# Kernel optimization log

Measured on AMD Instinct MI355X. Metric: run time of the kernel, lower is better.

The kernel has to match this reference:

```python
import jax, jax.numpy as jnp
import numpy as np
import math

SLEEP_DIM = 1024
BRAIN_DIM = 512
N_HEADS = 8
D_K = SLEEP_DIM // N_HEADS
N_S = 2048
N_C = 4096
LN_EPS = 1e-5


def setup_inputs() -> dict:
    key = jax.random.key(0)
    ks = jax.random.split(key, 9)
    s = 0.02  # weight init scale
    return {
        "H_S": jax.random.normal(ks[0], (N_S, SLEEP_DIM), dtype=jnp.float32),
        "H_C": jax.random.normal(ks[1], (N_C, BRAIN_DIM), dtype=jnp.float32),
        "G_glyph": jax.random.uniform(ks[2], (N_S, N_C), dtype=jnp.float32),
        "W_Q": jax.random.normal(ks[3], (SLEEP_DIM, SLEEP_DIM), dtype=jnp.float32) * s,
        "W_K": jax.random.normal(ks[4], (SLEEP_DIM, BRAIN_DIM), dtype=jnp.float32) * s,
        "W_V": jax.random.normal(ks[5], (SLEEP_DIM, BRAIN_DIM), dtype=jnp.float32) * s,
        "W_O": jax.random.normal(ks[6], (SLEEP_DIM, SLEEP_DIM), dtype=jnp.float32) * s,
        "b_O": jnp.zeros((SLEEP_DIM,), dtype=jnp.float32),
        "ln_gamma": jnp.ones((SLEEP_DIM,), dtype=jnp.float32),
        "ln_beta": jnp.zeros((SLEEP_DIM,), dtype=jnp.float32),
    }


def reference(H_S, H_C, G_glyph, W_Q, W_K, W_V, W_O, b_O, ln_gamma, ln_beta):
    # projections (torch Linear: x @ W.T)
    Q = (H_S @ W_Q.T).reshape(N_S, N_HEADS, D_K)   # (N_S, H, d_k)
    K = (H_C @ W_K.T).reshape(N_C, N_HEADS, D_K)   # (N_C, H, d_k)
    V = (H_C @ W_V.T).reshape(N_C, N_HEADS, D_K)   # (N_C, H, d_k)

    # scores: (N_S, N_C, H), scaled then multiplicatively gated per (s, c) pair
    scores = jnp.einsum("shd,chd->sch", Q, K) / math.sqrt(D_K)
    scores = scores * G_glyph[:, :, None]

    # softmax over keys (dim=1 of (N_S, N_C, H)); dropout is identity at eval
    attn = jax.nn.softmax(scores, axis=1)

    # weighted value sum, merge heads
    H_new = jnp.einsum("sch,chd->shd", attn, V).reshape(N_S, SLEEP_DIM)
    H_new = H_new @ W_O.T + b_O

    # residual + LayerNorm
    x = H_new + H_S
    mu = jnp.mean(x, axis=-1, keepdims=True)
    var = jnp.var(x, axis=-1, keepdims=True)
    out = (x - mu) / jnp.sqrt(var + LN_EPS) * ln_gamma + ln_beta
    return out, attn.mean(-1)
```

## Files before the change

### kernel.cpp

```cpp
#include <hip/hip_runtime.h>
#include <hip/hip_bf16.h>

#define NS 2048
#define NC 4096
#define SD 1024
#define BD 512
#define NH 8
#define DK 128

typedef __bf16 bf16;
typedef __bf16 bf16x8 __attribute__((ext_vector_type(8)));
typedef __bf16 bf16x4 __attribute__((ext_vector_type(4)));
typedef float f32x4 __attribute__((ext_vector_type(4)));

__device__ __forceinline__ bf16 f2bf(float f) { return (bf16)f; }
__device__ __forceinline__ bf16x8 ld8(const bf16* p) { return *(const bf16x8*)p; }
__device__ __forceinline__ f32x4 mfma16(bf16x8 a, bf16x8 b, f32x4 c) {
  return __builtin_amdgcn_mfma_f32_16x16x32_bf16(a, b, c, 0, 0, 0);
}

__global__ void k_cast(const float* __restrict__ in, bf16* __restrict__ out, int n4) {
  int i = blockIdx.x * blockDim.x + threadIdx.x;
  int stride = gridDim.x * blockDim.x;
  for (; i < n4; i += stride) {
    float4 v = ((const float4*)in)[i];
    bf16x4 o;
    o[0] = f2bf(v.x); o[1] = f2bf(v.y); o[2] = f2bf(v.z); o[3] = f2bf(v.w);
    ((bf16x4*)out)[i] = o;
  }
}

template <typename CT>
__global__ __launch_bounds__(256) void k_gemm_bt(const bf16* __restrict__ A,
                                                 const bf16* __restrict__ B,
                                                 CT* __restrict__ C,
                                                 int M, int N, int K) {
  __shared__ bf16 As[128 * 64];
  __shared__ bf16 Bs[64 * 64];
  const int tid = threadIdx.x;
  const int l = tid & 63, w = tid >> 6;
  const int g = l >> 4, r15 = l & 15;
  const int m0 = blockIdx.y * 128, n0 = blockIdx.x * 64;
  const int wm = (w >> 1) * 64, wn = (w & 1) * 32;
  f32x4 acc[4][2] = {};
  for (int k0 = 0; k0 < K; k0 += 64) {
    __syncthreads();
#pragma unroll
    for (int i = 0; i < 4; i++) {
      int slot = tid + i * 256;
      int row = slot >> 3, cp = slot & 7;
      int gc = cp ^ (row & 7);
      *(uint4*)(As + slot * 8) = *(const uint4*)(A + (size_t)(m0 + row) * K + k0 + gc * 8);
    }
#pragma unroll
    for (int i = 0; i < 2; i++) {
      int slot = tid + i * 256;
      int row = slot >> 3, cp = slot & 7;
      int gc = cp ^ (row & 7);
      *(uint4*)(Bs + slot * 8) = *(const uint4*)(B + (size_t)(n0 + row) * K + k0 + gc * 8);
    }
    __syncthreads();
#pragma unroll
    for (int kk = 0; kk < 2; kk++) {
      bf16x8 af[4], bfr[2];
#pragma unroll
      for (int mi = 0; mi < 4; mi++) {
        int row = wm + mi * 16 + r15;
        int cidx = (kk * 4 + g) ^ (row & 7);
        af[mi] = *(const bf16x8*)(As + row * 64 + cidx * 8);
      }
#pragma unroll
      for (int ni = 0; ni < 2; ni++) {
        int row = wn + ni * 16 + r15;
        int cidx = (kk * 4 + g) ^ (row & 7);
        bfr[ni] = *(const bf16x8*)(Bs + row * 64 + cidx * 8);
      }
#pragma unroll
      for (int mi = 0; mi < 4; mi++)
#pragma unroll
        for (int ni = 0; ni < 2; ni++)
          acc[mi][ni] = mfma16(af[mi], bfr[ni], acc[mi][ni]);
    }
  }
#pragma unroll
  for (int mi = 0; mi < 4; mi++)
#pragma unroll
    for (int ni = 0; ni < 2; ni++)
#pragma unroll
      for (int rr = 0; rr < 4; rr++) {
        int mrow = m0 + wm + mi * 16 + g * 4 + rr;
        int ncol = n0 + wn + ni * 16 + r15;
        float v = acc[mi][ni][rr];
        if constexpr (sizeof(CT) == 4) C[(size_t)mrow * N + ncol] = v;
        else                           C[(size_t)mrow * N + ncol] = f2bf(v);
      }
}

__global__ __launch_bounds__(256) void k_transpose(const bf16* __restrict__ V, bf16* __restrict__ Vt) {
  __shared__ bf16 tile[32][33];
  const int t = threadIdx.x;
  const int col = t & 31, r0 = t >> 5;
  const int cbase = blockIdx.y * 32;
  const int dbase = blockIdx.x * 32;
#pragma unroll
  for (int i = 0; i < 4; i++) {
    int r = r0 + i * 8;
    tile[r][col] = V[(size_t)(cbase + r) * SD + dbase + col];
  }
  __syncthreads();
#pragma unroll
  for (int i = 0; i < 4; i++) {
    int r = r0 + i * 8;
    Vt[(size_t)(dbase + r) * NC + cbase + col] = tile[col][r];
  }
}

__global__ __launch_bounds__(256) void k_attn2(const bf16* __restrict__ Q, const bf16* __restrict__ Km,
                                               const bf16* __restrict__ Vt, const float* __restrict__ Gf,
                                               float* __restrict__ psum_part, bf16* __restrict__ Opart) {
  __shared__ bf16 Kl[64 * 128];
  __shared__ bf16 Vl[128 * 64];
  __shared__ bf16 Pl[4][32 * 64];
  const int tid = threadIdx.x;
  const int l = tid & 63, w = tid >> 6;
  const int g = l >> 4, r15 = l & 15;
  const int s0 = blockIdx.x * 128;
  const int h = blockIdx.y, hoff = h * DK;
  const int ch = blockIdx.z;
  const int cbase = ch * (NC / 4);
  const float scale = 0.08838834764831845f;
  char* KlB = (char*)Kl;
  char* VlB = (char*)Vl;
  char* PlB = (char*)Pl[w];
  const int swz = r15 & 7;

  bf16x8 qf[2][4];
#pragma unroll
  for (int smi = 0; smi < 2; smi++)
#pragma unroll
    for (int kk = 0; kk < 4; kk++)
      qf[smi][kk] = ld8(Q + (size_t)(s0 + w * 32 + smi * 16 + r15) * SD + hoff + kk * 32 + g * 8);

  f32x4 oacc[8][2] = {};
  float psum[2] = {0.f, 0.f};

  const int krow0 = tid >> 4, ksl = tid & 15;
  const int vrow0 = tid >> 3, vsl = tid & 7;

  uint4 kreg[4], vreg[4];
  auto loadstep = [&](int cb) {
#pragma unroll
    for (int i = 0; i < 4; i++)
      kreg[i] = *(const uint4*)(Km + (size_t)(cb + krow0 + i * 16) * SD + hoff + ksl * 8);
#pragma unroll
    for (int i = 0; i < 4; i++)
      vreg[i] = *(const uint4*)(Vt + (size_t)(hoff + vrow0 + i * 32) * NC + cb + vsl * 8);
  };
  loadstep(cbase);

  for (int t = 0; t < 16; ++t) {
    const int cb = cbase + t * 64;
    __syncthreads();
#pragma unroll
    for (int i = 0; i < 4; i++) {
      int row = krow0 + i * 16;
      *(uint4*)(KlB + row * 256 + ((ksl ^ (row & 7)) << 4)) = kreg[i];
    }
#pragma unroll
    for (int i = 0; i < 4; i++) {
      int row = vrow0 + i * 32;
      *(uint4*)(VlB + row * 128 + ((vsl ^ (row & 7)) << 4)) = vreg[i];
    }
    __syncthreads();
    if (t < 15) loadstep(cb + 64);
#pragma unroll
    for (int csub = 0; csub < 4; ++csub) {
      bf16x8 kf[4];
#pragma unroll
      for (int kk = 0; kk < 4; kk++)
        kf[kk] = *(const bf16x8*)(KlB + (csub * 16 + r15) * 256 + (((kk * 4 + g) ^ swz) << 4));
#pragma unroll
      for (int smi = 0; smi < 2; smi++) {
        f32x4 a = {0.f, 0.f, 0.f, 0.f};
#pragma unroll
        for (int kk = 0; kk < 4; kk++) a = mfma16(kf[kk], qf[smi][kk], a);
        const int srow = s0 + w * 32 + smi * 16 + r15;
        float4 gv = *(const float4*)(Gf + (size_t)srow * NC + cb + csub * 16 + g * 4);
        float p0 = __expf(a[0] * scale * gv.x);
        float p1 = __expf(a[1] * scale * gv.y);
        float p2 = __expf(a[2] * scale * gv.z);
        float p3 = __expf(a[3] * scale * gv.w);
        psum[smi] += (p0 + p1) + (p2 + p3);
        bf16 pk[4] __attribute__((aligned(8)));
        pk[0] = f2bf(p0); pk[1] = f2bf(p1); pk[2] = f2bf(p2); pk[3] = f2bf(p3);
        *(uint2*)(PlB + (smi * 16 + r15) * 128 + ((csub * 32 + g * 8) ^ (swz << 4))) = *(const uint2*)pk;
      }
    }
#pragma unroll
    for (int kc = 0; kc < 2; ++kc) {
      bf16x8 pf[2];
#pragma unroll
      for (int smi = 0; smi < 2; smi++)
        pf[smi] = *(const bf16x8*)(PlB + (smi * 16 + r15) * 128 + ((kc * 64 + g * 16) ^ (swz << 4)));
#pragma unroll
      for (int nf = 0; nf < 8; ++nf) {
        bf16x8 vf = *(const bf16x8*)(VlB + (nf * 16 + r15) * 128 + (((kc * 4 + g) ^ swz) << 4));
#pragma unroll
        for (int smi = 0; smi < 2; smi++)
          oacc[nf][smi] = mfma16(vf, pf[smi], oacc[nf][smi]);
      }
    }
  }
#pragma unroll
  for (int smi = 0; smi < 2; smi++) {
    float ps = psum[smi];
    ps += __shfl_xor(ps, 16);
    ps += __shfl_xor(ps, 32);
    if (g == 0) {
      int srow = s0 + w * 32 + smi * 16 + r15;
      psum_part[((size_t)ch * NS + srow) * NH + h] = ps;
    }
  }
#pragma unroll
  for (int nf = 0; nf < 8; nf++)
#pragma unroll
    for (int smi = 0; smi < 2; smi++) {
      int srow = s0 + w * 32 + smi * 16 + r15;
      bf16 ob[4] __attribute__((aligned(8)));
#pragma unroll
      for (int rr = 0; rr < 4; rr++) ob[rr] = f2bf(oacc[nf][smi][rr]);
      *(uint2*)(Opart + ((size_t)ch * NS + srow) * SD + hoff + nf * 16 + g * 4) = *(const uint2*)ob;
    }
}

__global__ __launch_bounds__(256) void k_combine(const float* __restrict__ psum_part,
                                                 const bf16* __restrict__ Opart,
                                                 bf16* __restrict__ Hat, float* __restrict__ inv_l) {
  __shared__ float il_s[NH];
  const int row = blockIdx.x, t = threadIdx.x;
  if (t < NH) {
    float s = 0.f;
#pragma unroll
    for (int ch = 0; ch < 4; ch++) s += psum_part[((size_t)ch * NS + row) * NH + t];
    float iv = 1.0f / s;
    il_s[t] = iv;
    inv_l[(size_t)row * NH + t] = iv;
  }
  __syncthreads();
  const int d0 = t * 4;
  float acc[4] = {0.f, 0.f, 0.f, 0.f};
#pragma unroll
  for (int ch = 0; ch < 4; ch++) {
    bf16x4 v = *(const bf16x4*)(Opart + ((size_t)ch * NS + row) * SD + d0);
#pragma unroll
    for (int j = 0; j < 4; j++) acc[j] += (float)v[j];
  }
  float iv = il_s[d0 >> 7];
  bf16 ob[4] __attribute__((aligned(8)));
#pragma unroll
  for (int j = 0; j < 4; j++) ob[j] = f2bf(acc[j] * iv);
  *(uint2*)(Hat + (size_t)row * SD + d0) = *(const uint2*)ob;
}

__global__ __launch_bounds__(256) void k_mean2(const bf16* __restrict__ Q, const bf16* __restrict__ Km,
                                               const float* __restrict__ Gf, const float* __restrict__ inv_l,
                                               float* __restrict__ out_mean) {
  __shared__ bf16 Klm[64 * 128];
  __shared__ bf16 Qlm[64 * 128];
  const int tid = threadIdx.x;
  const int l = tid & 63, w = tid >> 6;
  const int g = l >> 4, r15 = l & 15;
  const int ws = w >> 1, wc = w & 1;
  const int c0 = blockIdx.x * 64, s0 = blockIdx.y * 64;
  const float scale = 0.08838834764831845f;
  const int swz = r15 & 7;
  char* KB = (char*)Klm;
  char* QB = (char*)Qlm;
  const int row0 = tid >> 4, sl = tid & 15;

  float4 gv[2][2];
#pragma unroll
  for (int smi = 0; smi < 2; smi++)
#pragma unroll
    for (int csub = 0; csub < 2; csub++)
      gv[smi][csub] = *(const float4*)(Gf + (size_t)(s0 + ws * 32 + smi * 16 + r15) * NC +
                                       c0 + wc * 32 + csub * 16 + g * 4);

  f32x4 macc[2][2] = {};
  uint4 kreg[4], qreg[4];
  auto loadh = [&](int h) {
#pragma unroll
    for (int i = 0; i < 4; i++)
      kreg[i] = *(const uint4*)(Km + (size_t)(c0 + row0 + i * 16) * SD + h * DK + sl * 8);
#pragma unroll
    for (int i = 0; i < 4; i++)
      qreg[i] = *(const uint4*)(Q + (size_t)(s0 + row0 + i * 16) * SD + h * DK + sl * 8);
  };
  loadh(0);
  for (int h = 0; h < NH; ++h) {
    __syncthreads();
#pragma unroll
    for (int i = 0; i < 4; i++) {
      int row = row0 + i * 16;
      *(uint4*)(KB + row * 256 + ((sl ^ (row & 7)) << 4)) = kreg[i];
    }
#pragma unroll
    for (int i = 0; i < 4; i++) {
      int row = row0 + i * 16;
      *(uint4*)(QB + row * 256 + ((sl ^ (row & 7)) << 4)) = qreg[i];
    }
    __syncthreads();
    if (h < NH - 1) loadh(h + 1);
    bf16x8 kf[2][4], qfr[2][4];
#pragma unroll
    for (int csub = 0; csub < 2; csub++)
#pragma unroll
      for (int kk = 0; kk < 4; kk++)
        kf[csub][kk] = *(const bf16x8*)(KB + (wc * 32 + csub * 16 + r15) * 256 + (((kk * 4 + g) ^ swz) << 4));
#pragma unroll
    for (int smi = 0; smi < 2; smi++)
#pragma unroll
      for (int kk = 0; kk < 4; kk++)
        qfr[smi][kk] = *(const bf16x8*)(QB + (ws * 32 + smi * 16 + r15) * 256 + (((kk * 4 + g) ^ swz) << 4));
    float ilv[2];
#pragma unroll
    for (int smi = 0; smi < 2; smi++)
      ilv[smi] = inv_l[(size_t)(s0 + ws * 32 + smi * 16 + r15) * NH + h];
#pragma unroll
    for (int smi = 0; smi < 2; smi++)
#pragma unroll
      for (int csub = 0; csub < 2; csub++) {
        f32x4 a = {0.f, 0.f, 0.f, 0.f};
#pragma unroll
        for (int kk = 0; kk < 4; kk++) a = mfma16(kf[csub][kk], qfr[smi][kk], a);
        float4 gvv = gv[smi][csub];
        macc[smi][csub][0] += __expf(a[0] * scale * gvv.x) * ilv[smi];
        macc[smi][csub][1] += __expf(a[1] * scale * gvv.y) * ilv[smi];
        macc[smi][csub][2] += __expf(a[2] * scale * gvv.z) * ilv[smi];
        macc[smi][csub][3] += __expf(a[3] * scale * gvv.w) * ilv[smi];
      }
  }
#pragma unroll
  for (int smi = 0; smi < 2; smi++)
#pragma unroll
    for (int csub = 0; csub < 2; csub++) {
      int srow = s0 + ws * 32 + smi * 16 + r15;
      float4 o;
      o.x = macc[smi][csub][0] * 0.125f;
      o.y = macc[smi][csub][1] * 0.125f;
      o.z = macc[smi][csub][2] * 0.125f;
      o.w = macc[smi][csub][3] * 0.125f;
      *(float4*)(out_mean + (size_t)srow * NC + c0 + wc * 32 + csub * 16 + g * 4) = o;
    }
}

__global__ __launch_bounds__(256) void k_ln(const float* __restrict__ Op, const float* __restrict__ HS,
                                            const float* __restrict__ bO, const float* __restrict__ gamma,
                                            const float* __restrict__ beta, float* __restrict__ out) {
  __shared__ float rs[4][2];
  const int row = blockIdx.x, t = threadIdx.x;
  const int l = t & 63, w = t >> 6;
  float4 xo = *(const float4*)(Op + (size_t)row * SD + t * 4);
  float4 hs = *(const float4*)(HS + (size_t)row * SD + t * 4);
  float4 bo = *(const float4*)(bO + t * 4);
  float x[4] = {xo.x + hs.x + bo.x, xo.y + hs.y + bo.y,
                xo.z + hs.z + bo.z, xo.w + hs.w + bo.w};
  float s = x[0] + x[1] + x[2] + x[3];
  float q = x[0] * x[0] + x[1] * x[1] + x[2] * x[2] + x[3] * x[3];
#pragma unroll
  for (int m = 1; m < 64; m <<= 1) { s += __shfl_xor(s, m); q += __shfl_xor(q, m); }
  if (l == 0) { rs[w][0] = s; rs[w][1] = q; }
  __syncthreads();
  s = rs[0][0] + rs[1][0] + rs[2][0] + rs[3][0];
  q = rs[0][1] + rs[1][1] + rs[2][1] + rs[3][1];
  float mean = s * (1.0f / SD);
  float var = q * (1.0f / SD) - mean * mean;
  float rstd = rsqrtf(var + 1e-5f);
  float4 gm = *(const float4*)(gamma + t * 4);
  float4 bt = *(const float4*)(beta + t * 4);
  float4 o;
  o.x = (x[0] - mean) * rstd * gm.x + bt.x;
  o.y = (x[1] - mean) * rstd * gm.y + bt.y;
  o.z = (x[2] - mean) * rstd * gm.z + bt.z;
  o.w = (x[3] - mean) * rstd * gm.w + bt.w;
  *(float4*)(out + (size_t)row * SD + t * 4) = o;
}

extern "C" void kernel_launch(void* const* d_in, const int* in_sizes, int n_in,
                              void* d_out, int out_size, void* d_ws, size_t ws_size,
                              hipStream_t stream) {
  const float* H_S = (const float*)d_in[0];
  const float* H_C = (const float*)d_in[1];
  const float* G   = (const float*)d_in[2];
  const float* W_Q = (const float*)d_in[3];
  const float* W_K = (const float*)d_in[4];
  const float* W_V = (const float*)d_in[5];
  const float* W_O = (const float*)d_in[6];
  const float* b_O = (const float*)d_in[7];
  const float* gam = (const float*)d_in[8];
  const float* bet = (const float*)d_in[9];
  float* out = (float*)d_out;
  float* out_mean = out + (size_t)NS * SD;

  char* p = (char*)d_ws;
  auto alloc = [&](size_t bytes) { char* r = p; p += (bytes + 255) & ~(size_t)255; return r; };
  char* region0 = alloc((size_t)20 << 20);
  bf16* HSb = (bf16*)region0;
  bf16* HCb = (bf16*)(region0 + ((size_t)4 << 20));
  bf16* WQb = (bf16*)(region0 + ((size_t)8 << 20));
  bf16* WKb = (bf16*)(region0 + ((size_t)10 << 20));
  bf16* WVb = (bf16*)(region0 + ((size_t)11 << 20));
  bf16* Vb  = (bf16*)(region0 + ((size_t)12 << 20));
  bf16* Opart = (bf16*)region0;
  bf16* WOb = (bf16*)alloc((size_t)SD * SD * 2);
  bf16* Qb  = (bf16*)alloc((size_t)NS * SD * 2);
  bf16* Kb  = (bf16*)alloc((size_t)NC * SD * 2);
  bf16* Vtb = (bf16*)alloc((size_t)SD * NC * 2);
  bf16* Hat = (bf16*)alloc((size_t)NS * SD * 2);
  float* Opj = (float*)alloc((size_t)NS * SD * 4);
  float* invl = (float*)alloc((size_t)NS * NH * 4);
  float* psum_part = (float*)alloc((size_t)4 * NS * NH * 4);

  k_cast<<<1024, 256, 0, stream>>>(H_S, HSb, NS * SD / 4);
  k_cast<<<1024, 256, 0, stream>>>(H_C, HCb, NC * BD / 4);
  k_cast<<<1024, 256, 0, stream>>>(W_Q, WQb, SD * SD / 4);
  k_cast<<<1024, 256, 0, stream>>>(W_K, WKb, SD * BD / 4);
  k_cast<<<1024, 256, 0, stream>>>(W_V, WVb, SD * BD / 4);
  k_cast<<<1024, 256, 0, stream>>>(W_O, WOb, SD * SD / 4);

  k_gemm_bt<bf16><<<dim3(SD / 64, NS / 128), 256, 0, stream>>>(HSb, WQb, Qb, NS, SD, SD);
  k_gemm_bt<bf16><<<dim3(SD / 64, NC / 128), 256, 0, stream>>>(HCb, WKb, Kb, NC, SD, BD);
  k_gemm_bt<bf16><<<dim3(SD / 64, NC / 128), 256, 0, stream>>>(HCb, WVb, Vb, NC, SD, BD);
  k_transpose<<<dim3(SD / 32, NC / 32), 256, 0, stream>>>(Vb, Vtb);

  k_attn2<<<dim3(NS / 128, NH, 4), 256, 0, stream>>>(Qb, Kb, Vtb, G, psum_part, Opart);
  k_combine<<<NS, 256, 0, stream>>>(psum_part, Opart, Hat, invl);
  k_mean2<<<dim3(NC / 64, NS / 64), 256, 0, stream>>>(Qb, Kb, G, invl, out_mean);

  k_gemm_bt<float><<<dim3(SD / 64, NS / 128), 256, 0, stream>>>(Hat, WOb, Opj, NS, SD, SD);
  k_ln<<<NS, 256, 0, stream>>>(Opj, H_S, b_O, gam, bet, out);
}
```

Baseline: 516.0 us.

## Fuse casts, cast G to bf16, shrink GEMM tiles, register-shuffle P in attention

Merges all input casts into one kernel and also casts the gating matrix G to bf16, so the attention and mean kernels read half the bytes for G. GEMM tiles shrink from 128x64 to 64x64 to give the grid more blocks. The attention kernel now has each wave handle 16 query rows, and it rearranges P into MFMA operand layout with cross-lane shuffles instead of an LDS round trip. Its output is staged through LDS so global stores are coalesced, and the mean kernel caches inv_l in shared memory. Rounding G to bf16 adds error to the gated scores, and the extra cast pass over G costs a full read of it plus a write of the bf16 copy.

Result: no change. 516.0 us (+0.0%).

```diff
diff --git a/kernel.cpp b/kernel.cpp
--- a/kernel.cpp
+++ b/kernel.cpp
@@ -7,46 +7,81 @@
 #define BD 512
 #define NH 8
 #define DK 128
+#define CSPLIT 4
 
 typedef __bf16 bf16;
 typedef __bf16 bf16x8 __attribute__((ext_vector_type(8)));
 typedef __bf16 bf16x4 __attribute__((ext_vector_type(4)));
 typedef float f32x4 __attribute__((ext_vector_type(4)));
+typedef unsigned u32x4 __attribute__((ext_vector_type(4)));
 
 __device__ __forceinline__ bf16 f2bf(float f) { return (bf16)f; }
 __device__ __forceinline__ bf16x8 ld8(const bf16* p) { return *(const bf16x8*)p; }
 __device__ __forceinline__ f32x4 mfma16(bf16x8 a, bf16x8 b, f32x4 c) {
   return __builtin_amdgcn_mfma_f32_16x16x32_bf16(a, b, c, 0, 0, 0);
 }
-
-__global__ void k_cast(const float* __restrict__ in, bf16* __restrict__ out, int n4) {
+__device__ __forceinline__ unsigned pkbf(float lo, float hi) {
+  unsigned short a = __builtin_bit_cast(unsigned short, (bf16)lo);
+  unsigned short b = __builtin_bit_cast(unsigned short, (bf16)hi);
+  return (unsigned)a | ((unsigned)b << 16);
+}
+
+__global__ void k_cast_all(const float* __restrict__ HS, const float* __restrict__ HC,
+                           const float* __restrict__ WQ, const float* __restrict__ WK,
+                           const float* __restrict__ WV, const float* __restrict__ WO,
+                           const float* __restrict__ G,
+                           bf16* __restrict__ HSb, bf16* __restrict__ HCb,
+                           bf16* __restrict__ WQb, bf16* __restrict__ WKb,
+                           bf16* __restrict__ WVb, bf16* __restrict__ WOb,
+                           bf16* __restrict__ Gb) {
+  const int n0 = NS * SD / 4, n1 = NC * BD / 4, n2 = SD * SD / 4, n3 = SD * BD / 4;
+  const int n4 = SD * BD / 4, n5 = SD * SD / 4, n6 = NS * NC / 4;
+  const int total = n0 + n1 + n2 + n3 + n4 + n5 + n6;
   int i = blockIdx.x * blockDim.x + threadIdx.x;
-  int stride = gridDim.x * blockDim.x;
-  for (; i < n4; i += stride) {
-    float4 v = ((const float4*)in)[i];
+  const int stride = gridDim.x * blockDim.x;
+  for (; i < total; i += stride) {
+    const float* s; bf16* d; int off = i;
+    if (off < n0) { s = HS; d = HSb; }
+    else { off -= n0;
+      if (off < n1) { s = HC; d = HCb; }
+      else { off -= n1;
+        if (off < n2) { s = WQ; d = WQb; }
+        else { off -= n2;
+          if (off < n3) { s = WK; d = WKb; }
+          else { off -= n3;
+            if (off < n4) { s = WV; d = WVb; }
+            else { off -= n4;
+              if (off < n5) { s = WO; d = WOb; }
+              else { off -= n5; s = G; d = Gb; }
+            }
+          }
+        }
+      }
+    }
+    float4 v = ((const float4*)s)[off];
     bf16x4 o;
     o[0] = f2bf(v.x); o[1] = f2bf(v.y); o[2] = f2bf(v.z); o[3] = f2bf(v.w);
-    ((bf16x4*)out)[i] = o;
+    ((bf16x4*)d)[off] = o;
   }
 }
 
 template <typename CT>
-__global__ __launch_bounds__(256) void k_gemm_bt(const bf16* __restrict__ A,
-                                                 const bf16* __restrict__ B,
-                                                 CT* __restrict__ C,
-                                                 int M, int N, int K) {
-  __shared__ bf16 As[128 * 64];
+__global__ __launch_bounds__(256) void k_gemm64(const bf16* __restrict__ A,
+                                                const bf16* __restrict__ B,
+                                                CT* __restrict__ C,
+                                                int M, int N, int K) {
+  __shared__ bf16 As[64 * 64];
   __shared__ bf16 Bs[64 * 64];
   const int tid = threadIdx.x;
   const int l = tid & 63, w = tid >> 6;
   const int g = l >> 4, r15 = l & 15;
-  const int m0 = blockIdx.y * 128, n0 = blockIdx.x * 64;
-  const int wm = (w >> 1) * 64, wn = (w & 1) * 32;
-  f32x4 acc[4][2] = {};
+  const int m0 = blockIdx.y * 64, n0 = blockIdx.x * 64;
+  const int wm = (w >> 1) * 32, wn = (w & 1) * 32;
+  f32x4 acc[2][2] = {};
   for (int k0 = 0; k0 < K; k0 += 64) {
     __syncthreads();
 #pragma unroll
-    for (int i = 0; i < 4; i++) {
+    for (int i = 0; i < 2; i++) {
       int slot = tid + i * 256;
       int row = slot >> 3, cp = slot & 7;
       int gc = cp ^ (row & 7);
@@ -62,9 +97,9 @@
     __syncthreads();
 #pragma unroll
     for (int kk = 0; kk < 2; kk++) {
-      bf16x8 af[4], bfr[2];
-#pragma unroll
-      for (int mi = 0; mi < 4; mi++) {
+      bf16x8 af[2], bfr[2];
+#pragma unroll
+      for (int mi = 0; mi < 2; mi++) {
         int row = wm + mi * 16 + r15;
         int cidx = (kk * 4 + g) ^ (row & 7);
         af[mi] = *(const bf16x8*)(As + row * 64 + cidx * 8);
@@ -76,14 +111,14 @@
         bfr[ni] = *(const bf16x8*)(Bs + row * 64 + cidx * 8);
       }
 #pragma unroll
-      for (int mi = 0; mi < 4; mi++)
+      for (int mi = 0; mi < 2; mi++)
 #pragma unroll
         for (int ni = 0; ni < 2; ni++)
           acc[mi][ni] = mfma16(af[mi], bfr[ni], acc[mi][ni]);
     }
   }
 #pragma unroll
-  for (int mi = 0; mi < 4; mi++)
+  for (int mi = 0; mi < 2; mi++)
 #pragma unroll
     for (int ni = 0; ni < 2; ni++)
 #pragma unroll
@@ -115,38 +150,31 @@
   }
 }
 
-__global__ __launch_bounds__(256) void k_attn2(const bf16* __restrict__ Q, const bf16* __restrict__ Km,
-                                               const bf16* __restrict__ Vt, const float* __restrict__ Gf,
-                                               float* __restrict__ psum_part, bf16* __restrict__ Opart) {
+__global__ __launch_bounds__(256, 4) void k_attn3(const bf16* __restrict__ Q, const bf16* __restrict__ Km,
+                                                  const bf16* __restrict__ Vt, const bf16* __restrict__ Gb,
+                                                  float* __restrict__ psum_part, bf16* __restrict__ Opart) {
   __shared__ bf16 Kl[64 * 128];
   __shared__ bf16 Vl[128 * 64];
-  __shared__ bf16 Pl[4][32 * 64];
-  const int tid = threadIdx.x;
-  const int l = tid & 63, w = tid >> 6;
-  const int g = l >> 4, r15 = l & 15;
-  const int s0 = blockIdx.x * 128;
+  const int tid = threadIdx.x, l = tid & 63, w = tid >> 6, g = l >> 4, r15 = l & 15;
+  const int s0 = blockIdx.x * 64;
   const int h = blockIdx.y, hoff = h * DK;
-  const int ch = blockIdx.z;
-  const int cbase = ch * (NC / 4);
+  const int ch = blockIdx.z, cbase = ch * (NC / CSPLIT);
+  const int srow = s0 + w * 16 + r15;
   const float scale = 0.08838834764831845f;
   char* KlB = (char*)Kl;
   char* VlB = (char*)Vl;
-  char* PlB = (char*)Pl[w];
   const int swz = r15 & 7;
 
-  bf16x8 qf[2][4];
-#pragma unroll
-  for (int smi = 0; smi < 2; smi++)
-#pragma unroll
-    for (int kk = 0; kk < 4; kk++)
-      qf[smi][kk] = ld8(Q + (size_t)(s0 + w * 32 + smi * 16 + r15) * SD + hoff + kk * 32 + g * 8);
-
-  f32x4 oacc[8][2] = {};
-  float psum[2] = {0.f, 0.f};
+  bf16x8 qf[4];
+#pragma unroll
+  for (int kk = 0; kk < 4; kk++)
+    qf[kk] = ld8(Q + (size_t)srow * SD + hoff + kk * 32 + g * 8);
+
+  f32x4 oacc[8] = {};
+  float psum = 0.f;
 
   const int krow0 = tid >> 4, ksl = tid & 15;
   const int vrow0 = tid >> 3, vsl = tid & 7;
-
   uint4 kreg[4], vreg[4];
   auto loadstep = [&](int cb) {
 #pragma unroll
@@ -158,7 +186,8 @@
   };
   loadstep(cbase);
 
-  for (int t = 0; t < 16; ++t) {
+  const int NT = NC / CSPLIT / 64;
+  for (int t = 0; t < NT; ++t) {
     const int cb = cbase + t * 64;
     __syncthreads();
 #pragma unroll
@@ -172,65 +201,78 @@
       *(uint4*)(VlB + row * 128 + ((vsl ^ (row & 7)) << 4)) = vreg[i];
     }
     __syncthreads();
-    if (t < 15) loadstep(cb + 64);
-#pragma unroll
-    for (int csub = 0; csub < 4; ++csub) {
-      bf16x8 kf[4];
-#pragma unroll
-      for (int kk = 0; kk < 4; kk++)
-        kf[kk] = *(const bf16x8*)(KlB + (csub * 16 + r15) * 256 + (((kk * 4 + g) ^ swz) << 4));
-#pragma unroll
-      for (int smi = 0; smi < 2; smi++) {
+    uint2 gcur[4];
+#pragma unroll
+    for (int cs = 0; cs < 4; cs++)
+      gcur[cs] = *(const uint2*)(Gb + (size_t)srow * NC + cb + cs * 16 + g * 4);
+    if (t < NT - 1) loadstep(cb + 64);
+#pragma unroll
+    for (int kc = 0; kc < 2; ++kc) {
+      unsigned va0, va1, vb0, vb1;
+#pragma unroll
+      for (int cs2 = 0; cs2 < 2; ++cs2) {
+        const int csub = kc * 2 + cs2;
+        bf16x8 kf[4];
+#pragma unroll
+        for (int kk = 0; kk < 4; kk++)
+          kf[kk] = *(const bf16x8*)(KlB + (csub * 16 + r15) * 256 + (((kk * 4 + g) ^ swz) << 4));
         f32x4 a = {0.f, 0.f, 0.f, 0.f};
 #pragma unroll
-        for (int kk = 0; kk < 4; kk++) a = mfma16(kf[kk], qf[smi][kk], a);
-        const int srow = s0 + w * 32 + smi * 16 + r15;
-        float4 gv = *(const float4*)(Gf + (size_t)srow * NC + cb + csub * 16 + g * 4);
-        float p0 = __expf(a[0] * scale * gv.x);
-        float p1 = __expf(a[1] * scale * gv.y);
-        float p2 = __expf(a[2] * scale * gv.z);
-        float p3 = __expf(a[3] * scale * gv.w);
-        psum[smi] += (p0 + p1) + (p2 + p3);
-        bf16 pk[4] __attribute__((aligned(8)));
-        pk[0] = f2bf(p0); pk[1] = f2bf(p1); pk[2] = f2bf(p2); pk[3] = f2bf(p3);
-        *(uint2*)(PlB + (smi * 16 + r15) * 128 + ((csub * 32 + g * 8) ^ (swz << 4))) = *(const uint2*)pk;
-      }
-    }
-#pragma unroll
-    for (int kc = 0; kc < 2; ++kc) {
-      bf16x8 pf[2];
-#pragma unroll
-      for (int smi = 0; smi < 2; smi++)
-        pf[smi] = *(const bf16x8*)(PlB + (smi * 16 + r15) * 128 + ((kc * 64 + g * 16) ^ (swz << 4)));
+        for (int kk = 0; kk < 4; kk++) a = mfma16(kf[kk], qf[kk], a);
+        bf16x4 gb4 = __builtin_bit_cast(bf16x4, gcur[csub]);
+        float p0 = __expf(a[0] * scale * (float)gb4[0]);
+        float p1 = __expf(a[1] * scale * (float)gb4[1]);
+        float p2 = __expf(a[2] * scale * (float)gb4[2]);
+        float p3 = __expf(a[3] * scale * (float)gb4[3]);
+        psum += (p0 + p1) + (p2 + p3);
+        if (cs2 == 0) { va0 = pkbf(p0, p1); va1 = pkbf(p2, p3); }
+        else          { vb0 = pkbf(p0, p1); vb1 = pkbf(p2, p3); }
+      }
+      const bool glow = (g < 2);
+      unsigned sa = glow ? vb0 : va0, sb = glow ? vb1 : va1;
+      unsigned e0 = (unsigned)__shfl_xor((int)sa, 32);
+      unsigned e1 = (unsigned)__shfl_xor((int)sb, 32);
+      unsigned p00 = glow ? va0 : e0, p01 = glow ? va1 : e1;
+      unsigned p10 = glow ? e0 : vb0, p11 = glow ? e1 : vb1;
+      const bool ge = ((g & 1) == 0);
+      unsigned t0 = ge ? p10 : p00, t1 = ge ? p11 : p01;
+      unsigned f0e = (unsigned)__shfl_xor((int)t0, 16);
+      unsigned f1e = (unsigned)__shfl_xor((int)t1, 16);
+      u32x4 fv;
+      fv[0] = ge ? p00 : f0e;
+      fv[1] = ge ? p01 : f1e;
+      fv[2] = ge ? f0e : p10;
+      fv[3] = ge ? f1e : p11;
+      bf16x8 pf = __builtin_bit_cast(bf16x8, fv);
 #pragma unroll
       for (int nf = 0; nf < 8; ++nf) {
         bf16x8 vf = *(const bf16x8*)(VlB + (nf * 16 + r15) * 128 + (((kc * 4 + g) ^ swz) << 4));
-#pragma unroll
-        for (int smi = 0; smi < 2; smi++)
-          oacc[nf][smi] = mfma16(vf, pf[smi], oacc[nf][smi]);
-      }
-    }
-  }
-#pragma unroll
-  for (int smi = 0; smi < 2; smi++) {
-    float ps = psum[smi];
-    ps += __shfl_xor(ps, 16);
-    ps += __shfl_xor(ps, 32);
-    if (g == 0) {
-      int srow = s0 + w * 32 + smi * 16 + r15;
-      psum_part[((size_t)ch * NS + srow) * NH + h] = ps;
-    }
-  }
-#pragma unroll
-  for (int nf = 0; nf < 8; nf++)
-#pragma unroll
-    for (int smi = 0; smi < 2; smi++) {
-      int srow = s0 + w * 32 + smi * 16 + r15;
-      bf16 ob[4] __attribute__((aligned(8)));
-#pragma unroll
-      for (int rr = 0; rr < 4; rr++) ob[rr] = f2bf(oacc[nf][smi][rr]);
-      *(uint2*)(Opart + ((size_t)ch * NS + srow) * SD + hoff + nf * 16 + g * 4) = *(const uint2*)ob;
-    }
+        oacc[nf] = mfma16(vf, pf, oacc[nf]);
+      }
+    }
+  }
+  float ps = psum;
+  ps += __shfl_xor(ps, 16);
+  ps += __shfl_xor(ps, 32);
+  if (g == 0) psum_part[((size_t)ch * NS + srow) * NH + h] = ps;
+
+  __syncthreads();
+  char* Sw = KlB + w * 4096;
+#pragma unroll
+  for (int nf = 0; nf < 8; ++nf) {
+    uint2 pk2;
+    pk2.x = pkbf(oacc[nf][0], oacc[nf][1]);
+    pk2.y = pkbf(oacc[nf][2], oacc[nf][3]);
+    *(uint2*)(Sw + r15 * 256 + ((nf * 32 + g * 8) ^ (swz << 4))) = pk2;
+  }
+  __syncthreads();
+  const int sr = l >> 2;
+#pragma unroll
+  for (int p = 0; p < 4; ++p) {
+    int cc = (l & 3) + p * 4;
+    uint4 v = *(const uint4*)(Sw + sr * 256 + ((cc * 16) ^ ((sr & 7) << 4)));
+    *(uint4*)(Opart + ((size_t)ch * NS + s0 + w * 16 + sr) * SD + hoff + cc * 8) = v;
+  }
 }
 
 __global__ __launch_bounds__(256) void k_combine(const float* __restrict__ psum_part,
@@ -241,7 +283,7 @@
   if (t < NH) {
     float s = 0.f;
 #pragma unroll
-    for (int ch = 0; ch < 4; ch++) s += psum_part[((size_t)ch * NS + row) * NH + t];
+    for (int ch = 0; ch < CSPLIT; ch++) s += psum_part[((size_t)ch * NS + row) * NH + t];
     float iv = 1.0f / s;
     il_s[t] = iv;
     inv_l[(size_t)row * NH + t] = iv;
@@ -250,7 +292,7 @@
   const int d0 = t * 4;
   float acc[4] = {0.f, 0.f, 0.f, 0.f};
 #pragma unroll
-  for (int ch = 0; ch < 4; ch++) {
+  for (int ch = 0; ch < CSPLIT; ch++) {
     bf16x4 v = *(const bf16x4*)(Opart + ((size_t)ch * NS + row) * SD + d0);
 #pragma unroll
     for (int j = 0; j < 4; j++) acc[j] += (float)v[j];
@@ -263,10 +305,11 @@
 }
 
 __global__ __launch_bounds__(256) void k_mean2(const bf16* __restrict__ Q, const bf16* __restrict__ Km,
-                                               const float* __restrict__ Gf, const float* __restrict__ inv_l,
+                                               const bf16* __restrict__ Gb, const float* __restrict__ inv_l,
                                                float* __restrict__ out_mean) {
   __shared__ bf16 Klm[64 * 128];
   __shared__ bf16 Qlm[64 * 128];
+  __shared__ float ilv_s[64][NH];
   const int tid = threadIdx.x;
   const int l = tid & 63, w = tid >> 6;
   const int g = l >> 4, r15 = l & 15;
@@ -278,12 +321,15 @@
   char* QB = (char*)Qlm;
   const int row0 = tid >> 4, sl = tid & 15;
 
-  float4 gv[2][2];
+  for (int i = tid; i < 64 * NH; i += 256)
+    ilv_s[i >> 3][i & 7] = inv_l[(size_t)(s0 + (i >> 3)) * NH + (i & 7)];
+
+  uint2 gvb[2][2];
 #pragma unroll
   for (int smi = 0; smi < 2; smi++)
 #pragma unroll
     for (int csub = 0; csub < 2; csub++)
-      gv[smi][csub] = *(const float4*)(Gf + (size_t)(s0 + ws * 32 + smi * 16 + r15) * NC +
+      gvb[smi][csub] = *(const uint2*)(Gb + (size_t)(s0 + ws * 32 + smi * 16 + r15) * NC +
                                        c0 + wc * 32 + csub * 16 + g * 4);
 
   f32x4 macc[2][2] = {};
@@ -325,7 +371,7 @@
     float ilv[2];
 #pragma unroll
     for (int smi = 0; smi < 2; smi++)
-      ilv[smi] = inv_l[(size_t)(s0 + ws * 32 + smi * 16 + r15) * NH + h];
+      ilv[smi] = ilv_s[ws * 32 + smi * 16 + r15][h];
 #pragma unroll
     for (int smi = 0; smi < 2; smi++)
 #pragma unroll
@@ -333,11 +379,11 @@
         f32x4 a = {0.f, 0.f, 0.f, 0.f};
 #pragma unroll
         for (int kk = 0; kk < 4; kk++) a = mfma16(kf[csub][kk], qfr[smi][kk], a);
-        float4 gvv = gv[smi][csub];
-        macc[smi][csub][0] += __expf(a[0] * scale * gvv.x) * ilv[smi];
-        macc[smi][csub][1] += __expf(a[1] * scale * gvv.y) * ilv[smi];
-        macc[smi][csub][2] += __expf(a[2] * scale * gvv.z) * ilv[smi];
-        macc[smi][csub][3] += __expf(a[3] * scale * gvv.w) * ilv[smi];
+        bf16x4 gb4 = __builtin_bit_cast(bf16x4, gvb[smi][csub]);
+        macc[smi][csub][0] += __expf(a[0] * scale * (float)gb4[0]) * ilv[smi];
+        macc[smi][csub][1] += __expf(a[1] * scale * (float)gb4[1]) * ilv[smi];
+        macc[smi][csub][2] += __expf(a[2] * scale * (float)gb4[2]) * ilv[smi];
+        macc[smi][csub][3] += __expf(a[3] * scale * (float)gb4[3]) * ilv[smi];
       }
   }
 #pragma unroll
@@ -419,24 +465,21 @@
   bf16* Hat = (bf16*)alloc((size_t)NS * SD * 2);
   float* Opj = (float*)alloc((size_t)NS * SD * 4);
   float* invl = (float*)alloc((size_t)NS * NH * 4);
-  float* psum_part = (float*)alloc((size_t)4 * NS * NH * 4);
-
-  k_cast<<<1024, 256, 0, stream>>>(H_S, HSb, NS * SD / 4);
-  k_cast<<<1024, 256, 0, stream>>>(H_C, HCb, NC * BD / 4);
-  k_cast<<<1024, 256, 0, stream>>>(W_Q, WQb, SD * SD / 4);
-  k_cast<<<1024, 256, 0, stream>>>(W_K, WKb, SD * BD / 4);
-  k_cast<<<1024, 256, 0, stream>>>(W_V, WVb, SD * BD / 4);
-  k_cast<<<1024, 256, 0, stream>>>(W_O, WOb, SD * SD / 4);
-
-  k_gemm_bt<bf16><<<dim3(SD / 64, NS / 128), 256, 0, stream>>>(HSb, WQb, Qb, NS, SD, SD);
-  k_gemm_bt<bf16><<<dim3(SD / 64, NC / 128), 256, 0, stream>>>(HCb, WKb, Kb, NC, SD, BD);
-  k_gemm_bt<bf16><<<dim3(SD / 64, NC / 128), 256, 0, stream>>>(HCb, WVb, Vb, NC, SD, BD);
+  float* psum_part = (float*)alloc((size_t)CSPLIT * NS * NH * 4);
+  bf16* Gb = (bf16*)alloc((size_t)NS * NC * 2);
+
+  k_cast_all<<<2048, 256, 0, stream>>>(H_S, H_C, W_Q, W_K, W_V, W_O, G,
+                                       HSb, HCb, WQb, WKb, WVb, WOb, Gb);
+
+  k_gemm64<bf16><<<dim3(SD / 64, NS / 64), 256, 0, stream>>>(HSb, WQb, Qb, NS, SD, SD);
+  k_gemm64<bf16><<<dim3(SD / 64, NC / 64), 256, 0, stream>>>(HCb, WKb, Kb, NC, SD, BD);
+  k_gemm64<bf16><<<dim3(SD / 64, NC / 64), 256, 0, stream>>>(HCb, WVb, Vb, NC, SD, BD);
   k_transpose<<<dim3(SD / 32, NC / 32), 256, 0, stream>>>(Vb, Vtb);
 
-  k_attn2<<<dim3(NS / 128, NH, 4), 256, 0, stream>>>(Qb, Kb, Vtb, G, psum_part, Opart);
+  k_attn3<<<dim3(NS / 64, NH, CSPLIT), 256, 0, stream>>>(Qb, Kb, Vtb, Gb, psum_part, Opart);
   k_combine<<<NS, 256, 0, stream>>>(psum_part, Opart, Hat, invl);
-  k_mean2<<<dim3(NC / 64, NS / 64), 256, 0, stream>>>(Qb, Kb, G, invl, out_mean);
-
-  k_gemm_bt<float><<<dim3(SD / 64, NS / 128), 256, 0, stream>>>(Hat, WOb, Opj, NS, SD, SD);
+  k_mean2<<<dim3(NC / 64, NS / 64), 256, 0, stream>>>(Qb, Kb, Gb, invl, out_mean);
+
+  k_gemm64<float><<<dim3(SD / 64, NS / 64), 256, 0, stream>>>(Hat, WOb, Opj, NS, SD, SD);
   k_ln<<<NS, 256, 0, stream>>>(Opj, H_S, b_O, gam, bet, out);
 }
```
